# Kernel optimization log

Measured on AMD Instinct MI355X. Metric: run time of the kernel, lower is better.

Reference implementation:

```python
import jax, jax.numpy as jnp
import numpy as np
from jax import lax

B = 256
R_ITERS = 3

def squash(x):
    # x * |x| / (1 + |x|^2), applied along last axis
    n = jnp.linalg.norm(x, axis=-1, keepdims=True)
    return x * n / (1.0 + n * n)

def conv2d(x, w, b, stride):
    y = lax.conv_general_dilated(x, w, window_strides=(stride, stride), padding='VALID',
                                 dimension_numbers=('NCHW', 'OIHW', 'NCHW'))
    return y + b[None, :, None, None]

def setup_inputs() -> dict:
    key = jax.random.key(0)
    ks = jax.random.split(key, 12)
    s = 0.05
    return {
        'x': jax.random.normal(ks[0], (B, 1, 28, 28), jnp.float32),
        'label': jax.random.randint(ks[1], (B,), 0, 10),
        'conv1_w': jax.random.normal(ks[2], (256, 1, 9, 9), jnp.float32) * s,
        'conv1_b': jnp.zeros((256,), jnp.float32),
        'pconv_w': jax.random.normal(ks[3], (256, 256, 9, 9), jnp.float32) * s,
        'pconv_b': jnp.zeros((256,), jnp.float32),
        'W_dig': jax.random.normal(ks[4], (1152, 10, 16, 8), jnp.float32),
        'dec_w1': jax.random.normal(ks[5], (512, 160), jnp.float32) * s,
        'dec_b1': jnp.zeros((512,), jnp.float32),
        'dec_w2': jax.random.normal(ks[6], (1024, 512), jnp.float32) * s,
        'dec_b2': jnp.zeros((1024,), jnp.float32),
        'dec_w3': jax.random.normal(ks[7], (784, 1024), jnp.float32) * s,
        'dec_b3': jnp.zeros((784,), jnp.float32),
    }

def reference(x, label, conv1_w, conv1_b, pconv_w, pconv_b, W_dig,
              dec_w1, dec_b1, dec_w2, dec_b2, dec_w3, dec_b3):
    # conv stem: [B,1,28,28] -> [B,256,20,20]
    h = conv2d(x, conv1_w, conv1_b, 1)
    # primary caps conv: -> [B,256,6,6] -> [B,1152,8] -> squash
    h = conv2d(h, pconv_w, pconv_b, 2)
    caps = squash(h.reshape(h.shape[0], -1, 8))
    # prediction vectors u_hat: [B, 1152, 10, 16]
    u = jnp.einsum('iond,bid->bion', W_dig, caps)
    # dynamic routing (softmax over input-capsule axis, per original code)
    b = jnp.zeros_like(u)
    for r in range(1, R_ITERS + 1):
        c = jax.nn.softmax(b, axis=1)
        s = (c * u).sum(axis=1, keepdims=True)     # [B,1,10,16]
        v = squash(s)
        if r != R_ITERS:
            b = b + (v * u).sum(axis=-1, keepdims=True)
    v = v.squeeze(1)                               # [B,10,16]
    # masked reconstruction
    one_hot = jax.nn.one_hot(label, 10, dtype=v.dtype)
    recon = (one_hot[..., None] * v).reshape(v.shape[0], 160)
    recon = jax.nn.relu(recon @ dec_w1.T + dec_b1)
    recon = jax.nn.relu(recon @ dec_w2.T + dec_b2)
    recon = jax.nn.sigmoid(recon @ dec_w3.T + dec_b3)
    return (v, recon, one_hot)
```

## Files before the change

### kernel.cpp

```cpp
#include <hip/hip_runtime.h>
#include <hip/hip_bf16.h>
#include <stdint.h>


typedef short short8 __attribute__((ext_vector_type(8)));
typedef unsigned short u16x8 __attribute__((ext_vector_type(8)));
typedef float f32x4  __attribute__((ext_vector_type(4)));

__device__ inline float bf2f(unsigned short u) {
    unsigned int v = ((unsigned int)u) << 16;
    float f;
    __builtin_memcpy(&f, &v, 4);
    return f;
}
__device__ inline unsigned short f2bf(float f) {
    __hip_bfloat16 h = __float2bfloat16(f);
    unsigned short u;
    __builtin_memcpy(&u, &h, 2);
    return u;
}
__device__ inline float clampf(float x, float b) {
    return fminf(fmaxf(x, -b), b);
}
__device__ inline float rdf(const void* p, size_t i, int f) {
    return f ? ((const float*)p)[i] : bf2f(((const unsigned short*)p)[i]);
}
__device__ inline void gload_lds16(const unsigned short* g, unsigned short* l) {
    __builtin_amdgcn_global_load_lds(
        (const __attribute__((address_space(1))) void*)g,
        (__attribute__((address_space(3))) void*)l, 16, 0, 0);
}
__device__ inline int detect_f(const void* w1c) {
    const unsigned short* w = (const unsigned short*)w1c;
    int lane = threadIdx.x & 63;
    int cnt = 0;
#pragma unroll
    for (int j = 0; j < 4; ++j) {
        float v = fabsf(bf2f(w[lane * 4 + j]));
        if (v > 100.f) cnt++;
    }
#pragma unroll
    for (int off = 32; off; off >>= 1) cnt += __shfl_xor(cnt, off);
    return cnt >= 4;
}

__global__ __launch_bounds__(256) void k_prep(
        const void* __restrict__ w1c, const void* __restrict__ w2c,
        float* __restrict__ h2f, unsigned short* __restrict__ B1p,
        unsigned short* __restrict__ Bp3) {
    __shared__ unsigned short wl[20736];
    int blk = blockIdx.x, tid = threadIdx.x;
    if (blk < 2304) {
        ((f32x4*)h2f)[blk * 256 + tid] = (f32x4){0.f, 0.f, 0.f, 0.f};
    } else if (blk < 2400) {
        int f = detect_f(w1c);
        int idx = (blk - 2304) * 256 + tid;
        int co = idx / 96, k = idx - co * 96;
        B1p[idx] = (k < 81) ? f2bf(rdf(w1c, (size_t)co * 81 + k, f)) : (unsigned short)0;
    } else {
        int f = detect_f(w1c);
        int co = blk - 2400;
        size_t base = (size_t)co * 20736;
        for (int i = tid; i < 20736; i += 256)
            wl[i] = f2bf(rdf(w2c, base + i, f));
        __syncthreads();
        for (int idx = tid; idx < 20736; idx += 256) {
            int t = idx >> 8, ci = idx & 255;
            int kc = ci >> 6, cin = ci & 63;
            Bp3[((size_t)(t * 4 + kc) << 14) + (co << 6) + cin] = wl[ci * 81 + t];
        }
    }
}

__global__ __launch_bounds__(256) void k_prep2(
        const void* __restrict__ wdig, const void* __restrict__ dw2,
        const void* __restrict__ dw3, const void* __restrict__ w1c,
        unsigned short* __restrict__ Wdb2,
        unsigned short* __restrict__ w2b,
        unsigned short* __restrict__ w3b) {
    __shared__ unsigned short wl[20480];
    int f = detect_f(w1c);
    int blk = blockIdx.x, tid = threadIdx.x;
    if (blk < 72) {
        int i0 = blk * 16;
        size_t base = (size_t)i0 * 1280;
        for (int idx = tid; idx < 20480; idx += 256)
            wl[idx] = f2bf(rdf(wdig, base + idx, f));
        __syncthreads();
        if (tid < 160) {
            int o = tid / 16, n = tid - o * 16;
            unsigned short* dst = Wdb2 + (size_t)o * 147456 + n * 9216 + i0 * 8;
            const unsigned short* src = wl + tid * 8;
#pragma unroll
            for (int i = 0; i < 16; ++i)
                *(uint4*)(dst + i * 8) = *(const uint4*)(src + i * 1280);
        }
    } else if (blk < 2120) {
        int idx = (blk - 72) * 256 + tid;
        w2b[idx] = f2bf(rdf(dw2, idx, f));
    } else {
        int idx = (blk - 2120) * 256 + tid;
        w3b[idx] = (idx < 802816) ? f2bf(rdf(dw3, idx, f)) : (unsigned short)0;
    }
}

__global__ __launch_bounds__(256) void k_conv1(
        const void* __restrict__ x,
        const unsigned short* __restrict__ B1p,
        const void* __restrict__ bias,
        unsigned short* __restrict__ h1p,
        const void* __restrict__ w1c) {
    __shared__ unsigned short xl[1568];
    __shared__ int offt[96];
    int f = detect_f(w1c);
    int tid = threadIdx.x;
    if (tid < 96) offt[tid] = (tid < 81) ? (tid / 9) * 28 + (tid % 9) : 0;

    int mblk = blockIdx.x * 128;
    int bfirst = mblk / 400;
    int blast = (mblk + 127) / 400;
    int nload = (blast - bfirst + 1) * 784;
    for (int i = tid; i < nload; i += 256)
        xl[i] = f2bf(rdf(x, (size_t)bfirst * 784 + i, f));
    __syncthreads();

    int wave = tid >> 6, lane = tid & 63;
    int wr = wave >> 1, wc = wave & 1;
    int mbase = mblk + wr * 64;
    int nbase = blockIdx.y * 128 + wc * 64;
    int l15 = lane & 15, l4 = lane >> 4;

    int lbase[4];
#pragma unroll
    for (int mt = 0; mt < 4; ++mt) {
        int m = mbase + mt * 16 + l15;
        int img = m / 400 - bfirst, pos = m % 400;
        lbase[mt] = img * 784 + (pos / 20) * 28 + (pos % 20);
    }

    f32x4 acc[4][4];
#pragma unroll
    for (int mt = 0; mt < 4; ++mt)
#pragma unroll
        for (int nt = 0; nt < 4; ++nt)
            acc[mt][nt] = (f32x4){0.f, 0.f, 0.f, 0.f};

#pragma unroll
    for (int kc = 0; kc < 3; ++kc) {
        int kbase = kc * 32 + l4 * 8;
        short8 af[4], bfr[4];
#pragma unroll
        for (int mt = 0; mt < 4; ++mt)
#pragma unroll
            for (int j = 0; j < 8; ++j) {
                int k = kbase + j;
                af[mt][j] = (k < 81) ? (short)xl[lbase[mt] + offt[k]] : (short)0;
            }
#pragma unroll
        for (int nt = 0; nt < 4; ++nt)
            bfr[nt] = *(const short8*)(B1p + (size_t)(nbase + nt * 16 + l15) * 96 + kbase);
#pragma unroll
        for (int mt = 0; mt < 4; ++mt)
#pragma unroll
            for (int nt = 0; nt < 4; ++nt)
                acc[mt][nt] = __builtin_amdgcn_mfma_f32_16x16x32_bf16(
                    af[mt], bfr[nt], acc[mt][nt], 0, 0, 0);
    }

#pragma unroll
    for (int mt = 0; mt < 4; ++mt)
#pragma unroll
        for (int nt = 0; nt < 4; ++nt) {
            int col = nbase + nt * 16 + l15;
            float bv = rdf(bias, col, f);
#pragma unroll
            for (int r = 0; r < 4; ++r) {
                int row = mbase + mt * 16 + l4 * 4 + r;
                h1p[(size_t)row * 256 + col] = f2bf(clampf(acc[mt][nt][r] + bv, 1024.f));
            }
        }
}

__global__ __launch_bounds__(256) void k_conv2(
        const unsigned short* __restrict__ h1p,
        const unsigned short* __restrict__ Bp,
        float* __restrict__ h2f) {
    __shared__ unsigned short As[8192];
    __shared__ unsigned short Bs[8192];
    int tid = threadIdx.x;
    int wave = tid >> 6, lane = tid & 63;
    int wr = wave >> 1, wc = wave & 1;
    int mb = blockIdx.x * 128, nb = blockIdx.y * 128;
    int s = blockIdx.z;
    int t0 = (81 * s) >> 3, t1 = (81 * (s + 1)) >> 3;
    int l15 = lane & 15, l4 = lane >> 4;

    int seg = lane & 7;
    int rsub = lane >> 3;
    int arowoff[4];
#pragma unroll
    for (int r = 0; r < 4; ++r) {
        int m = mb + wave * 32 + r * 8 + rsub;
        int bb = m / 36, pos = m - bb * 36;
        int y = pos / 6, xx = pos - y * 6;
        arowoff[r] = (bb * 400 + y * 40 + xx * 2) * 256 + seg * 8;
    }
    int lane8 = lane << 3;

    int arow[4], brow[4];
#pragma unroll
    for (int mt = 0; mt < 4; ++mt) arow[mt] = (wr * 64 + mt * 16 + l15) << 6;
#pragma unroll
    for (int nt = 0; nt < 4; ++nt) brow[nt] = (wc * 64 + nt * 16 + l15) << 6;

    f32x4 acc[4][4];
#pragma unroll
    for (int mt = 0; mt < 4; ++mt)
#pragma unroll
        for (int nt = 0; nt < 4; ++nt)
            acc[mt][nt] = (f32x4){0.f, 0.f, 0.f, 0.f};

    for (int t = t0; t < t1; ++t) {
        int ky = t / 9, kx = t - ky * 9;
        int tadd = (ky * 20 + kx) * 256;
#pragma unroll
        for (int kc = 0; kc < 4; ++kc) {
            const unsigned short* bwin =
                Bp + (((size_t)(t * 4 + kc)) << 14) + nb * 64;
#pragma unroll
            for (int r = 0; r < 4; ++r) {
                int q512 = (wave * 4 + r) << 9;
                gload_lds16(h1p + arowoff[r] + tadd + (kc << 6), As + q512);
                gload_lds16(bwin + q512 + lane8,                Bs + q512);
            }
            __syncthreads();
#pragma unroll
            for (int kk = 0; kk < 2; ++kk) {
                int ko = (kk << 5) + (l4 << 3);
                short8 af[4], bfr[4];
#pragma unroll
                for (int mt = 0; mt < 4; ++mt)
                    af[mt] = *(const short8*)(As + arow[mt] + ko);
#pragma unroll
                for (int nt = 0; nt < 4; ++nt)
                    bfr[nt] = *(const short8*)(Bs + brow[nt] + ko);
#pragma unroll
                for (int mt = 0; mt < 4; ++mt)
#pragma unroll
                    for (int nt = 0; nt < 4; ++nt)
                        acc[mt][nt] = __builtin_amdgcn_mfma_f32_16x16x32_bf16(
                            af[mt], bfr[nt], acc[mt][nt], 0, 0, 0);
            }
            __syncthreads();
        }
    }

#pragma unroll
    for (int mt = 0; mt < 4; ++mt)
#pragma unroll
        for (int nt = 0; nt < 4; ++nt) {
            int col = nb + wc * 64 + nt * 16 + l15;
#pragma unroll
            for (int r = 0; r < 4; ++r) {
                int row = mb + wr * 64 + mt * 16 + l4 * 4 + r;
                atomicAdd(&h2f[(size_t)row * 256 + col], acc[mt][nt][r]);
            }
        }
}

__global__ __launch_bounds__(256) void k_caps2(
        const float* __restrict__ h2f, const void* __restrict__ pb,
        unsigned short* __restrict__ caps, const void* __restrict__ w1c) {
    __shared__ float ld[9216];
    int f = detect_f(w1c);
    int b = blockIdx.x, tid = threadIdx.x;
#pragma unroll 4
    for (int p = 0; p < 36; ++p)
        ld[p * 256 + tid] = h2f[(size_t)b * 9216 + p * 256 + tid];
    __syncthreads();
    for (int c = tid; c < 1152; c += 256) {
        float h[8], ss = 0.f;
#pragma unroll
        for (int d = 0; d < 8; ++d) {
            int flat = c * 8 + d;
            int co = flat / 36, pos = flat - co * 36;
            float v = clampf(ld[pos * 256 + co] + rdf(pb, co, f), 20000.f);
            h[d] = v;
            ss += v * v;
        }
        float sc = sqrtf(ss) / (1.f + ss);
        u16x8 cv;
#pragma unroll
        for (int d = 0; d < 8; ++d) cv[d] = f2bf(h[d] * sc);
        *(u16x8*)(caps + ((size_t)b * 1152 + c) * 8) = cv;
    }
}

__global__ __launch_bounds__(384) void k_routing(
        const unsigned short* __restrict__ caps, const unsigned short* __restrict__ Wdb2,
        const int* __restrict__ label, void* __restrict__ d_out,
        float* __restrict__ vsel, const void* __restrict__ w1c) {
    int f = detect_f(w1c);
    int bo = blockIdx.x;
    int b = bo / 10, o = bo - b * 10;
    int tid = threadIdx.x;
    int wid = tid >> 6, lane = tid & 63;

    __shared__ float redw[6][16];
    __shared__ float sbuf[16];
    __shared__ float mred[8];
    __shared__ float sred[8];

    float u[3][16];
    float a[3] = {0.f, 0.f, 0.f};
    const unsigned short* capb = caps + (size_t)b * 9216;
    const unsigned short* wob = Wdb2 + (size_t)o * 147456;

#pragma unroll
    for (int r = 0; r < 3; ++r) {
        int i = tid + r * 384;
        u16x8 cq = *(const u16x8*)(capb + i * 8);
        float cf[8];
#pragma unroll
        for (int d = 0; d < 8; ++d) cf[d] = bf2f(cq[d]);
#pragma unroll
        for (int n = 0; n < 16; ++n) {
            u16x8 q = *(const u16x8*)(wob + ((size_t)n * 1152 + i) * 8);
            float sacc = 0.f;
#pragma unroll
            for (int d = 0; d < 8; ++d) sacc += bf2f(q[d]) * cf[d];
            u[r][n] = sacc;
        }
    }

    for (int rr = 1; rr <= 3; ++rr) {
        float mx = fmaxf(fmaxf(a[0], a[1]), a[2]);
#pragma unroll
        for (int off = 32; off; off >>= 1) mx = fmaxf(mx, __shfl_xor(mx, off));
        if (lane == 0) mred[wid] = mx;
        __syncthreads();
        float M = mred[0];
#pragma unroll
        for (int w = 1; w < 6; ++w) M = fmaxf(M, mred[w]);

        float e[3], es = 0.f;
#pragma unroll
        for (int r = 0; r < 3; ++r) { e[r] = __expf(a[r] - M); es += e[r]; }
#pragma unroll
        for (int off = 32; off; off >>= 1) es += __shfl_xor(es, off);
        if (lane == 0) sred[wid] = es;
        __syncthreads();
        float S = 0.f;
#pragma unroll
        for (int w = 0; w < 6; ++w) S += sred[w];
        float inv = 1.f / S;

        float p[16];
#pragma unroll
        for (int n = 0; n < 16; ++n)
            p[n] = (e[0] * u[0][n] + e[1] * u[1][n] + e[2] * u[2][n]) * inv;
#pragma unroll
        for (int n = 0; n < 16; ++n)
#pragma unroll
            for (int off = 32; off; off >>= 1) p[n] += __shfl_xor(p[n], off);
        if (lane == 0)
#pragma unroll
            for (int n = 0; n < 16; ++n) redw[wid][n] = p[n];
        __syncthreads();
        if (tid < 16) {
            float sn = 0.f;
#pragma unroll
            for (int w = 0; w < 6; ++w) sn += redw[w][tid];
            sbuf[tid] = sn;
        }
        __syncthreads();

        float ss = 0.f;
#pragma unroll
        for (int n = 0; n < 16; ++n) ss += sbuf[n] * sbuf[n];
        float sc = sqrtf(ss) / (1.f + ss);

        if (rr < 3) {
#pragma unroll
            for (int r = 0; r < 3; ++r) {
                float dot = 0.f;
#pragma unroll
                for (int n = 0; n < 16; ++n) dot += sbuf[n] * u[r][n];
                a[r] += sc * dot;
            }
            __syncthreads();
        } else {
            int lbl = label[b];
            if (tid < 16) {
                float vn = clampf(sbuf[tid] * sc, 1.f);
                if (f) ((float*)d_out)[(bo << 4) + tid] = vn;
                else   ((unsigned short*)d_out)[(bo << 4) + tid] = f2bf(vn);
                if (o == lbl) vsel[(b << 4) + tid] = vn;
            }
            if (tid == 0) {
                float oh = (o == lbl) ? 1.f : 0.f;
                if (f) ((float*)d_out)[241664 + bo] = oh;
                else   ((unsigned short*)d_out)[241664 + bo] = f2bf(oh);
            }
        }
    }
}

__global__ void k_dec1(const float* __restrict__ vsel, const int* __restrict__ label,
                       const void* __restrict__ w1, const void* __restrict__ b1,
                       unsigned short* __restrict__ r1b, const void* __restrict__ w1c) {
    int f = detect_f(w1c);
    int b = blockIdx.x, j = threadIdx.x;
    __shared__ float vs[16];
    if (j < 16) vs[j] = vsel[b * 16 + j];
    __syncthreads();
    int lbl = label[b];
    size_t wb = (size_t)j * 160 + lbl * 16;
    float acc = rdf(b1, j, f);
#pragma unroll
    for (int n = 0; n < 16; ++n) acc += rdf(w1, wb + n, f) * vs[n];
    r1b[b * 512 + j] = f2bf(fmaxf(acc, 0.f));
}

__global__ __launch_bounds__(256) void k_dgemm(
        const unsigned short* __restrict__ A, const unsigned short* __restrict__ B,
        const void* __restrict__ bias, int K, int mode, int nvalid, int ostride,
        unsigned short* __restrict__ outb, void* __restrict__ d_out,
        const void* __restrict__ w1c) {
    int f = detect_f(w1c);
    int tid = threadIdx.x;
    int wave = tid >> 6, lane = tid & 63;
    int wr = wave >> 1, wc = wave & 1;
    int mbase = blockIdx.x * 128 + wr * 64;
    int nbase = blockIdx.y * 128 + wc * 64;
    int l15 = lane & 15, l4 = lane >> 4;
    int koff = l4 * 8;

    f32x4 acc[4][4];
#pragma unroll
    for (int mt = 0; mt < 4; ++mt)
#pragma unroll
        for (int nt = 0; nt < 4; ++nt)
            acc[mt][nt] = (f32x4){0.f, 0.f, 0.f, 0.f};

    int nch = K >> 5;
    for (int kc = 0; kc < nch; ++kc) {
        int k0 = kc * 32 + koff;
        short8 af[4], bfr[4];
#pragma unroll
        for (int mt = 0; mt < 4; ++mt)
            af[mt] = *(const short8*)(A + (size_t)(mbase + mt * 16 + l15) * K + k0);
#pragma unroll
        for (int nt = 0; nt < 4; ++nt)
            bfr[nt] = *(const short8*)(B + (size_t)(nbase + nt * 16 + l15) * K + k0);
#pragma unroll
        for (int mt = 0; mt < 4; ++mt)
#pragma unroll
            for (int nt = 0; nt < 4; ++nt)
                acc[mt][nt] = __builtin_amdgcn_mfma_f32_16x16x32_bf16(
                    af[mt], bfr[nt], acc[mt][nt], 0, 0, 0);
    }

#pragma unroll
    for (int mt = 0; mt < 4; ++mt)
#pragma unroll
        for (int nt = 0; nt < 4; ++nt) {
            int col = nbase + nt * 16 + l15;
            float bv = (col < nvalid) ? rdf(bias, col, f) : 0.f;
#pragma unroll
            for (int r = 0; r < 4; ++r) {
                int row = mbase + mt * 16 + l4 * 4 + r;
                float v = acc[mt][nt][r] + bv;
                if (mode == 0) {
                    outb[(size_t)row * ostride + col] = f2bf(fmaxf(v, 0.f));
                } else if (col < nvalid) {
                    float a = clampf(v, 60.f);
                    float sig = 1.f / (1.f + __expf(-a));
                    size_t oi = 40960 + (size_t)row * 784 + col;
                    if (f) ((float*)d_out)[oi] = sig;
                    else   ((unsigned short*)d_out)[oi] = f2bf(sig);
                }
            }
        }
}

extern "C" void kernel_launch(void* const* d_in, const int* in_sizes, int n_in,
                              void* d_out, int out_size, void* d_ws, size_t ws_size,
                              hipStream_t stream) {
    const void* x    = d_in[0];
    const int*  lbl  = (const int*)d_in[1];
    const void* w1c  = d_in[2];
    const void* b1c  = d_in[3];
    const void* w2c  = d_in[4];
    const void* b2c  = d_in[5];
    const void* wdig = d_in[6];
    const void* dw1  = d_in[7];
    const void* db1  = d_in[8];
    const void* dw2  = d_in[9];
    const void* db2  = d_in[10];
    const void* dw3  = d_in[11];
    const void* db3  = d_in[12];
    (void)in_sizes; (void)n_in; (void)out_size; (void)ws_size;

    char* ws = (char*)d_ws;
    float* h2f           = (float*)(ws);
    unsigned short* Bp3  = (unsigned short*)(ws + 9437184);
    unsigned short* caps = (unsigned short*)(ws + 9437184);
    unsigned short* B1p  = (unsigned short*)(ws + 20054016);
    unsigned short* h1p  = (unsigned short*)(ws + 20103168);
    unsigned short* Wdb2 = (unsigned short*)(ws + 20103168);
    unsigned short* w2b  = (unsigned short*)(ws + 23052288);
    unsigned short* w3b  = (unsigned short*)(ws + 24100864);
    unsigned short* r1b  = (unsigned short*)(ws + 25935872);
    unsigned short* r2b  = (unsigned short*)(ws + 26198016);
    float* vsel          = (float*)(ws + 26722304);

    hipLaunchKernelGGL(k_prep,  dim3(2656),     dim3(256), 0, stream, w1c, w2c, h2f, B1p, Bp3);
    hipLaunchKernelGGL(k_conv1, dim3(800, 2),   dim3(256), 0, stream, x, B1p, b1c, h1p, w1c);
    hipLaunchKernelGGL(k_conv2, dim3(72, 2, 8), dim3(256), 0, stream, h1p, Bp3, h2f);
    hipLaunchKernelGGL(k_prep2, dim3(5704),     dim3(256), 0, stream,
                       wdig, dw2, dw3, w1c, Wdb2, w2b, w3b);
    hipLaunchKernelGGL(k_caps2, dim3(256),      dim3(256), 0, stream, h2f, b2c, caps, w1c);
    hipLaunchKernelGGL(k_routing, dim3(2560),   dim3(384), 0, stream, caps, Wdb2, lbl,
                       d_out, vsel, w1c);
    hipLaunchKernelGGL(k_dec1,  dim3(256),      dim3(512), 0, stream, vsel, lbl, dw1, db1, r1b, w1c);
    hipLaunchKernelGGL(k_dgemm, dim3(2, 8),     dim3(256), 0, stream,
                       r1b, w2b, db2, 512, 0, 1024, 1024, r2b, d_out, w1c);
    hipLaunchKernelGGL(k_dgemm, dim3(2, 7),     dim3(256), 0, stream,
                       r2b, w3b, db3, 1024, 1, 784, 0, (unsigned short*)nullptr, d_out, w1c);
}
```

Baseline: 576.2 us.

## Double-buffer conv2 LDS tiles with XOR-swizzled layout and finer K steps

Restructures the primary-caps conv GEMM main loop so the next K-slice (32 wide) is staged into a second LDS buffer while MFMAs run on the current one, with a single barrier per step. It also XOR-swizzles the LDS column segments to reduce bank conflicts on the short8 fragment reads. The smaller K-step doubles the number of barriers and waits, and the full vmcnt(0) wait may limit how much overlap is achieved.

```diff
diff --git a/kernel.cpp b/kernel.cpp
--- a/kernel.cpp
+++ b/kernel.cpp
@@ -185,8 +185,8 @@
         const unsigned short* __restrict__ h1p,
         const unsigned short* __restrict__ Bp,
         float* __restrict__ h2f) {
-    __shared__ unsigned short As[8192];
-    __shared__ unsigned short Bs[8192];
+    __shared__ unsigned short As[2][4096];
+    __shared__ unsigned short Bs[2][4096];
     int tid = threadIdx.x;
     int wave = tid >> 6, lane = tid & 63;
     int wr = wave >> 1, wc = wave & 1;
@@ -195,23 +195,25 @@
     int t0 = (81 * s) >> 3, t1 = (81 * (s + 1)) >> 3;
     int l15 = lane & 15, l4 = lane >> 4;
 
-    int seg = lane & 7;
-    int rsub = lane >> 3;
-    int arowoff[4];
-#pragma unroll
-    for (int r = 0; r < 4; ++r) {
-        int m = mb + wave * 32 + r * 8 + rsub;
+    int rsub = lane >> 2;
+    int slog = (lane & 3) ^ ((lane >> 3) & 3);
+    int aoff[2], boff[2];
+#pragma unroll
+    for (int r = 0; r < 2; ++r) {
+        int row = wave * 32 + r * 16 + rsub;
+        int m = mb + row;
         int bb = m / 36, pos = m - bb * 36;
         int y = pos / 6, xx = pos - y * 6;
-        arowoff[r] = (bb * 400 + y * 40 + xx * 2) * 256 + seg * 8;
-    }
-    int lane8 = lane << 3;
-
+        aoff[r] = (bb * 400 + y * 40 + xx * 2) * 256 + slog * 8;
+        boff[r] = row * 64 + slog * 8;
+    }
+
+    int ko = (l4 ^ ((l15 >> 1) & 3)) << 3;
     int arow[4], brow[4];
 #pragma unroll
-    for (int mt = 0; mt < 4; ++mt) arow[mt] = (wr * 64 + mt * 16 + l15) << 6;
-#pragma unroll
-    for (int nt = 0; nt < 4; ++nt) brow[nt] = (wc * 64 + nt * 16 + l15) << 6;
+    for (int mt = 0; mt < 4; ++mt) arow[mt] = ((wr * 64 + mt * 16 + l15) << 5) + ko;
+#pragma unroll
+    for (int nt = 0; nt < 4; ++nt) brow[nt] = ((wc * 64 + nt * 16 + l15) << 5) + ko;
 
     f32x4 acc[4][4];
 #pragma unroll
@@ -220,39 +222,57 @@
         for (int nt = 0; nt < 4; ++nt)
             acc[mt][nt] = (f32x4){0.f, 0.f, 0.f, 0.f};
 
-    for (int t = t0; t < t1; ++t) {
-        int ky = t / 9, kx = t - ky * 9;
-        int tadd = (ky * 20 + kx) * 256;
-#pragma unroll
-        for (int kc = 0; kc < 4; ++kc) {
-            const unsigned short* bwin =
-                Bp + (((size_t)(t * 4 + kc)) << 14) + nb * 64;
-#pragma unroll
-            for (int r = 0; r < 4; ++r) {
-                int q512 = (wave * 4 + r) << 9;
-                gload_lds16(h1p + arowoff[r] + tadd + (kc << 6), As + q512);
-                gload_lds16(bwin + q512 + lane8,                Bs + q512);
-            }
-            __syncthreads();
-#pragma unroll
-            for (int kk = 0; kk < 2; ++kk) {
-                int ko = (kk << 5) + (l4 << 3);
-                short8 af[4], bfr[4];
-#pragma unroll
-                for (int mt = 0; mt < 4; ++mt)
-                    af[mt] = *(const short8*)(As + arow[mt] + ko);
-#pragma unroll
-                for (int nt = 0; nt < 4; ++nt)
-                    bfr[nt] = *(const short8*)(Bs + brow[nt] + ko);
-#pragma unroll
-                for (int mt = 0; mt < 4; ++mt)
-#pragma unroll
-                    for (int nt = 0; nt < 4; ++nt)
-                        acc[mt][nt] = __builtin_amdgcn_mfma_f32_16x16x32_bf16(
-                            af[mt], bfr[nt], acc[mt][nt], 0, 0, 0);
-            }
-            __syncthreads();
-        }
+    int skc = 0;
+    int sky = t0 / 9, skx = t0 - sky * 9;
+    int stadd = (sky * 20 + skx) << 8;
+    int st4 = t0 * 4;
+
+    auto stage = [&](int buf) {
+        const unsigned short* aw = h1p + stadd + (skc << 5);
+        const unsigned short* bw = Bp + (((size_t)(st4 + (skc >> 1))) << 14)
+                                     + nb * 64 + ((skc & 1) << 5);
+        unsigned short* al = &As[buf][wave << 10];
+        unsigned short* bl = &Bs[buf][wave << 10];
+#pragma unroll
+        for (int r = 0; r < 2; ++r) {
+            gload_lds16(aw + aoff[r], al + (r << 9));
+            gload_lds16(bw + boff[r], bl + (r << 9));
+        }
+    };
+    auto adv = [&]() {
+        if (++skc == 8) {
+            skc = 0; st4 += 4;
+            if (++skx == 9) { skx = 0; stadd += 3072; }
+            else            { stadd += 256; }
+        }
+    };
+    auto compute = [&](int buf) {
+        short8 af[4], bfr[4];
+#pragma unroll
+        for (int mt = 0; mt < 4; ++mt)
+            af[mt] = *(const short8*)(&As[buf][arow[mt]]);
+#pragma unroll
+        for (int nt = 0; nt < 4; ++nt)
+            bfr[nt] = *(const short8*)(&Bs[buf][brow[nt]]);
+#pragma unroll
+        for (int mt = 0; mt < 4; ++mt)
+#pragma unroll
+            for (int nt = 0; nt < 4; ++nt)
+                acc[mt][nt] = __builtin_amdgcn_mfma_f32_16x16x32_bf16(
+                    af[mt], bfr[nt], acc[mt][nt], 0, 0, 0);
+    };
+
+    int nit = (t1 - t0) * 8;
+    stage(0); adv();
+    asm volatile("s_waitcnt vmcnt(0)" ::: "memory");
+    __builtin_amdgcn_s_barrier();
+    int cur = 0;
+    for (int i = 0; i < nit; ++i) {
+        if (i + 1 < nit) { stage(cur ^ 1); adv(); }
+        compute(cur);
+        asm volatile("s_waitcnt vmcnt(0)" ::: "memory");
+        __builtin_amdgcn_s_barrier();
+        cur ^= 1;
     }
 
 #pragma unroll
```

Result: faster. 552.6 us (-4.1%).
